# Kernel tuning notes

Hardware: AMD Instinct MI355X
Metric: run time of the kernel (lower is better)

## Reference

```python
import jax, jax.numpy as jnp
import numpy as np

B = 2; L = 64; HOP = 256; T = L * HOP
IN_CH = 101; INNER = 128; COND = 81
NBLOCK = 2; LAYERS = 5; K = 3; KH = 64
COUT = 2 * INNER
KCH = INNER * COUT * K * LAYERS   # 491520
BCH = COUT * LAYERS               # 1280


def setup_inputs() -> dict:
    key = jax.random.key(0)
    ks = jax.random.split(key, 12)
    n = lambda k, s, sc: jax.random.normal(k, s, jnp.float32) * sc
    return {
        "x": n(ks[0], (B, IN_CH, T), 1.0),
        "c": n(ks[1], (B, COND, L), 1.0),
        "fc_W": n(ks[2], (INNER, IN_CH), 0.1),
        "fc_b": jnp.zeros((INNER,), jnp.float32),
        "inp_W": n(ks[3], (NBLOCK, KH, COND, 5), 0.05),
        "inp_b": jnp.zeros((NBLOCK, KH), jnp.float32),
        "res1_W": n(ks[4], (NBLOCK, KH, KH), 0.1),
        "res1_b": jnp.zeros((NBLOCK, KH), jnp.float32),
        "res2_W": n(ks[5], (NBLOCK, KH, KH), 0.1),
        "res2_b": jnp.zeros((NBLOCK, KH), jnp.float32),
        "kern_W": n(ks[6], (NBLOCK, KCH, KH), 0.02),
        "kern_b": jnp.zeros((NBLOCK, KCH), jnp.float32),
        "biasc_W": n(ks[7], (NBLOCK, BCH, KH), 0.02),
        "biasc_b": jnp.zeros((NBLOCK, BCH), jnp.float32),
        "lc1_W": n(ks[8], (INNER, INNER), 0.08),
        "lc1_b": jnp.zeros((INNER,), jnp.float32),
        "lc2_W": n(ks[9], (1, INNER), 0.08),
        "lc2_b": jnp.zeros((1,), jnp.float32),
    }


def _conv1x1(x, W, b):
    return jnp.einsum('oc,bcl->bol', W, x) + b[None, :, None]


def _conv5(x, W, b):
    y = jax.lax.conv_general_dilated(x, W, (1,), [(2, 2)],
                                     dimension_numbers=('NCH', 'OIH', 'NCH'))
    return y + b[None, :, None]


def _lrelu(x):
    return jnp.where(x >= 0, x, 0.1 * x)


def _kernel_predictor(c, iW, ib, r1W, r1b, r2W, r2b, kW, kb, bW, bb):
    h = _lrelu(_conv5(c, iW, ib))
    h = h + _conv1x1(_lrelu(_conv1x1(h, r1W, r1b)), r2W, r2b)
    k = _conv1x1(h, kW, kb)   # (B, KCH, L)
    bb_ = _conv1x1(h, bW, bb)  # (B, BCH, L)
    Bn, _, Ln = c.shape
    kernels = k.reshape(Bn, LAYERS, INNER, COUT, K, Ln)
    bias = bb_.reshape(Bn, LAYERS, COUT, Ln)
    return kernels, bias


def _lvc(x, kernel, bias, dilation, hop):
    # x: (B, Cin, T); kernel: (B, Cin, Cout, K, L); bias: (B, Cout, L)
    Bn, Cin, Tn = x.shape
    _, _, O, Kn, Ln = kernel.shape
    p = dilation * (Kn - 1) // 2
    xp = jnp.pad(x, ((0, 0), (0, 0), (p, p)))
    win = hop + 2 * p
    # per-window gather (unfold over time with stride hop)
    idx = (jnp.arange(Ln) * hop)[:, None] + jnp.arange(win)[None, :]
    xw = xp[:, :, idx]
    m = win // dilation                                  # hop/d + (K-1)
    xt = xw.reshape(Bn, Cin, Ln, m, dilation).transpose(0, 1, 2, 4, 3)  # (B,Cin,L,d,m)
    S = hop // dilation
    idx2 = jnp.arange(S)[:, None] + jnp.arange(Kn)[None, :]  # (S, K) sliding taps
    xu = xt[..., idx2]                                   # (B, Cin, L, d, S, K)
    o = jnp.einsum('bildsk,biokl->bolsd', xu, kernel)
    o = o + bias[:, :, :, None, None]
    return o.reshape(Bn, O, Tn)


def _lvc_block(x, c, iW, ib, r1W, r1b, r2W, r2b, kW, kb, bW, bb):
    kernels, bias = _kernel_predictor(c, iW, ib, r1W, r1b, r2W, r2b, kW, kb, bW, bb)
    for i in range(LAYERS):
        d = 2 ** i  # max 16 < hop, so hop<dilation branch never triggers
        y = _lvc(x, kernels[:, i], bias[:, i], d, HOP)
        x = jax.nn.sigmoid(y[:, :INNER]) * jnp.tanh(y[:, INNER:])
    return x


def reference(x, c, fc_W, fc_b, inp_W, inp_b, res1_W, res1_b, res2_W, res2_b,
              kern_W, kern_b, biasc_W, biasc_b, lc1_W, lc1_b, lc2_W, lc2_b):
    h = _conv1x1(x, fc_W, fc_b)
    for n_ in range(NBLOCK):
        y = _lvc_block(h, c, inp_W[n_], inp_b[n_], res1_W[n_], res1_b[n_],
                       res2_W[n_], res2_b[n_], kern_W[n_], kern_b[n_],
                       biasc_W[n_], biasc_b[n_])
        h = y if n_ == 0 else h + y
    h = jnp.maximum(h, 0.0)
    h = _conv1x1(h, lc1_W, lc1_b)
    h = jnp.maximum(h, 0.0)
    h = _conv1x1(h, lc2_W, lc2_b)
    return h
```

## Files before the change

kernel.cpp:

```cpp
#include <hip/hip_runtime.h>
#include <math.h>

#define BB     2
#define LSEG   64
#define HOP    256
#define TT     (LSEG*HOP)
#define IN_CH  101
#define INNER  128
#define COND   81
#define LAYERS 5
#define KTAP   3
#define KH     64
#define COUT   256
#define RPL    (INNER*COUT*KTAP)
#define KCH    (RPL*LAYERS)
#define BCH    (COUT*LAYERS)
#define NBL    (BB*LSEG)
#define XS     36

typedef _Float16 f16;
typedef _Float16 f16x2 __attribute__((ext_vector_type(2)));
typedef _Float16 f16x8 __attribute__((ext_vector_type(8)));
typedef float    f32x4 __attribute__((ext_vector_type(4)));

__global__ __launch_bounds__(256) void k_fc(const float* __restrict__ x,
                                            const float* __restrict__ W,
                                            const float* __restrict__ bias,
                                            f16* __restrict__ out) {
    int half = blockIdx.x & 1;
    int g = (blockIdx.x >> 1)*256 + threadIdx.x;
    int b = g / TT, t = g % TT;
    float xv[IN_CH];
    const float* xp = x + (size_t)b*IN_CH*TT + t;
#pragma unroll
    for (int c = 0; c < IN_CH; ++c) xv[c] = xp[(size_t)c*TT];
    f16* op = out + (size_t)b*INNER*TT + t;
    int o0 = half*64;
    for (int o = o0; o < o0 + 64; ++o) {
        const float* wr = W + o*IN_CH;
        float a0 = bias[o], a1 = 0.f, a2 = 0.f, a3 = 0.f;
#pragma unroll
        for (int c = 0; c + 3 < IN_CH; c += 4) {
            a0 += wr[c]*xv[c]; a1 += wr[c+1]*xv[c+1];
            a2 += wr[c+2]*xv[c+2]; a3 += wr[c+3]*xv[c+3];
        }
        a0 += wr[100]*xv[100];
        op[(size_t)o*TT] = (f16)((a0+a1)+(a2+a3));
    }
}

__global__ __launch_bounds__(256) void k_h1(const float* __restrict__ cc,
                                            const float* __restrict__ iW,
                                            const float* __restrict__ ib,
                                            float* __restrict__ h1buf) {
    int og = blockIdx.x & 7;
    int bp = blockIdx.x >> 3;
    int b  = bp & 1;
    int n  = bp >> 1;
    __shared__ float cL[COND*LSEG];
    __shared__ float wL[8*COND*5];
    int tid = threadIdx.x;
    for (int idx = tid; idx < COND*LSEG; idx += 256)
        cL[idx] = cc[(size_t)b*COND*LSEG + idx];
    const float* wsrc = iW + (size_t)n*KH*COND*5 + (size_t)og*8*COND*5;
    for (int idx = tid; idx < 8*COND*5; idx += 256)
        wL[idx] = wsrc[idx];
    __syncthreads();
#pragma unroll
    for (int rep = 0; rep < 2; ++rep) {
        int idx = rep*256 + tid;
        int ol = idx >> 6, l = idx & 63;
        int o  = og*8 + ol;
        float acc = ib[n*KH + o];
        const float* wrow = wL + ol*COND*5;
        for (int i = 0; i < COND; ++i) {
            const float* crow = cL + i*LSEG;
            const float* w5 = wrow + i*5;
#pragma unroll
            for (int k = 0; k < 5; ++k) {
                int ll = l + k - 2;
                if (ll >= 0 && ll < LSEG) acc += crow[ll]*w5[k];
            }
        }
        h1buf[(((size_t)(n*BB + b))*KH + o)*LSEG + l] = acc >= 0.f ? acc : 0.1f*acc;
    }
}

__global__ __launch_bounds__(256) void k_h2t(const float* __restrict__ h1buf,
                                             const float* __restrict__ r1W,
                                             const float* __restrict__ r1b,
                                             const float* __restrict__ r2W,
                                             const float* __restrict__ r2b,
                                             float* __restrict__ h2buf,
                                             f16* __restrict__ h2h) {
    int b = blockIdx.x & 1;
    int n = blockIdx.x >> 1;
    __shared__ float h1L[KH*LSEG];
    __shared__ float t1L[KH*LSEG];
    __shared__ float wL[KH*KH];
    int tid = threadIdx.x;
    const float* h1src = h1buf + ((size_t)(n*BB + b))*KH*LSEG;
    for (int idx = tid; idx < KH*LSEG; idx += 256)
        h1L[idx] = h1src[idx];
    for (int idx = tid; idx < KH*KH; idx += 256)
        wL[idx] = r1W[(size_t)n*KH*KH + idx];
    __syncthreads();
#pragma unroll
    for (int rep = 0; rep < 16; ++rep) {
        int idx = rep*256 + tid;
        int o = idx >> 6, l = idx & 63;
        float acc = r1b[n*KH + o];
        const float* wr = wL + o*KH;
#pragma unroll
        for (int i = 0; i < KH; ++i) acc += wr[i]*h1L[i*LSEG + l];
        t1L[idx] = acc >= 0.f ? acc : 0.1f*acc;
    }
    __syncthreads();
    for (int idx = tid; idx < KH*KH; idx += 256)
        wL[idx] = r2W[(size_t)n*KH*KH + idx];
    __syncthreads();
#pragma unroll
    for (int rep = 0; rep < 16; ++rep) {
        int idx = rep*256 + tid;
        int o = idx >> 6, l = idx & 63;
        float acc = r2b[n*KH + o];
        const float* wr = wL + o*KH;
#pragma unroll
        for (int i = 0; i < KH; ++i) acc += wr[i]*t1L[i*LSEG + l];
        float h2 = h1L[o*LSEG + l] + acc;
        size_t row = (size_t)n*NBL + b*LSEG + l;
        h2buf[row*KH + o] = h2;
        h2h  [row*KH + o] = (f16)h2;
    }
}

__global__ __launch_bounds__(256) void k_biash(const float* __restrict__ bW,
                                               const float* __restrict__ bb,
                                               const float* __restrict__ h2buf,
                                               float* __restrict__ biasbuf) {
    int tg = blockIdx.x*256 + threadIdx.x;
    int n  = __builtin_amdgcn_readfirstlane(tg / (BB*BCH));
    int rem = tg - n*(BB*BCH);
    int b  = __builtin_amdgcn_readfirstlane(rem / BCH);
    int rb = rem % BCH;
    float w[KH];
    const float4* wp = (const float4*)(bW + ((size_t)n*BCH + rb)*KH);
#pragma unroll
    for (int q = 0; q < KH/4; ++q) {
        float4 v = wp[q];
        w[4*q] = v.x; w[4*q+1] = v.y; w[4*q+2] = v.z; w[4*q+3] = v.w;
    }
    float bv = bb[n*BCH + rb];
    for (int l = 0; l < LSEG; ++l) {
        size_t row = (size_t)n*NBL + b*LSEG + l;
        const float* h2 = h2buf + row*KH;
        float a0 = bv, a1 = 0.f, a2 = 0.f, a3 = 0.f;
#pragma unroll
        for (int j = 0; j < KH; j += 4) {
            a0 += w[j]*h2[j]; a1 += w[j+1]*h2[j+1];
            a2 += w[j+2]*h2[j+2]; a3 += w[j+3]*h2[j+3];
        }
        biasbuf[row*BCH + rb] = (a0+a1)+(a2+a3);
    }
}

__global__ __launch_bounds__(256) void k_gen(const float* __restrict__ kW,
                                             const float* __restrict__ kb,
                                             const f16*   __restrict__ h2h,
                                             f16*         __restrict__ kbuf) {
    int o2  = blockIdx.x & 127;
    int tmp = blockIdx.x >> 7;
    int tap = tmp % 3;
    int tmp2 = tmp / 3;
    int lay = tmp2 % 5;
    int n   = tmp2 / 5;
    int c   = threadIdx.x & 127;
    int oh  = threadIdx.x >> 7;
    int o   = o2 + (oh << 7);
    size_t r = (size_t)lay*RPL + (size_t)((c*COUT + o)*KTAP + tap);
    f16x2 wh[32];
    const float4* wp = (const float4*)(kW + ((size_t)n*KCH + r)*KH);
#pragma unroll
    for (int q = 0; q < 16; ++q) {
        float4 v = wp[q];
        wh[2*q]   = f16x2{(f16)v.x, (f16)v.y};
        wh[2*q+1] = f16x2{(f16)v.z, (f16)v.w};
    }
    float kbv = kb[(size_t)n*KCH + r];
    int op = 2*o2 + oh;
    size_t obase = (size_t)op*384 + (size_t)tap*128 + c;
    f16* kout = kbuf + ((size_t)(n*LAYERS + lay)*NBL)*RPL + obase;
    const uint* h2p = (const uint*)(h2h + (size_t)n*NBL*KH);
#pragma unroll 2
    for (int bl = 0; bl < NBL; ++bl) {
        const uint* hr = h2p + bl*32;
        float a0 = kbv, a1 = 0.f, a2 = 0.f, a3 = 0.f;
#pragma unroll
        for (int q = 0; q < 8; ++q) {
            a0 = __builtin_amdgcn_fdot2(wh[4*q],   __builtin_bit_cast(f16x2, hr[4*q]),   a0, false);
            a1 = __builtin_amdgcn_fdot2(wh[4*q+1], __builtin_bit_cast(f16x2, hr[4*q+1]), a1, false);
            a2 = __builtin_amdgcn_fdot2(wh[4*q+2], __builtin_bit_cast(f16x2, hr[4*q+2]), a2, false);
            a3 = __builtin_amdgcn_fdot2(wh[4*q+3], __builtin_bit_cast(f16x2, hr[4*q+3]), a3, false);
        }
        kout[(size_t)bl*RPL] = (f16)((a0+a1)+(a2+a3));
    }
}

template<int DIL>
__global__ __launch_bounds__(256) void k_lvc(const f16* __restrict__ xin,
                                             const f16* __restrict__ kbuf,
                                             const float* __restrict__ biasbuf,
                                             f16* __restrict__ xout,
                                             int layerIdx) {
    constexpr int WIN = 256 + 2*DIL;
    int wg  = blockIdx.x;
    int o0  = (wg & 3)*64;
    int l   = (wg >> 2) & 63;
    int b   = wg >> 8;
    int bl  = b*LSEG + l;
    int tid = threadIdx.x;
    int w   = tid >> 6;
    int lane = tid & 63;
    int quad = lane >> 4;
    int n16  = lane & 15;
    int wo = (w & 1)*32;
    int wt = (w >> 1)*128;

    __shared__ f16 As[3*64*XS];
    __shared__ f16 xwin[288*XS];

    const float* bias_l = biasbuf + (size_t)bl*BCH + layerIdx*COUT;
    f32x4 acc[2][8];
#pragma unroll
    for (int j = 0; j < 2; ++j) {
        int g0 = (o0 + wo + j*16 + quad*4) >> 1;
        f32x4 ini;
        ini[0] = bias_l[g0];       ini[1] = bias_l[g0 + 128];
        ini[2] = bias_l[g0 + 1];   ini[3] = bias_l[g0 + 1 + 128];
#pragma unroll
        for (int tt = 0; tt < 8; ++tt) acc[j][tt] = ini;
    }

    const f16* xb = xin + (size_t)b*INNER*TT;
    const f16* kbl = kbuf + (size_t)bl*RPL + (size_t)o0*384;
    int o_l = tid >> 2, q4 = tid & 3;
    int gt0 = l*256 - DIL;

    for (int cb = 0; cb < 4; ++cb) {
        for (int cc = w; cc < 32; cc += 4) {
            const f16* src = xb + (size_t)(cb*32 + cc)*TT;
#pragma unroll
            for (int tw0 = 0; tw0 < WIN; tw0 += 64) {
                int tw = tw0 + lane;
                if (tw < WIN) {
                    int gt = gt0 + tw;
                    f16 v = ((unsigned)gt < (unsigned)TT) ? src[gt] : (f16)0.f;
                    xwin[tw*XS + cc] = v;
                }
            }
        }
#pragma unroll
        for (int tap = 0; tap < 3; ++tap) {
            f16x8 v = *(const f16x8*)&kbl[(size_t)o_l*384 + tap*128 + cb*32 + q4*8];
            *(f16x8*)&As[(tap*64 + o_l)*XS + q4*8] = v;
        }
        __syncthreads();
#pragma unroll
        for (int tap = 0; tap < 3; ++tap) {
            f16x8 af0 = *(const f16x8*)&As[(tap*64 + wo + n16)*XS + quad*8];
            f16x8 af1 = *(const f16x8*)&As[(tap*64 + wo + 16 + n16)*XS + quad*8];
#pragma unroll
            for (int tt = 0; tt < 8; ++tt) {
                int trow = wt + tt*16 + n16 + tap*DIL;
                f16x8 bf = *(const f16x8*)&xwin[trow*XS + quad*8];
                acc[0][tt] = __builtin_amdgcn_mfma_f32_16x16x32_f16(af0, bf, acc[0][tt], 0, 0, 0);
                acc[1][tt] = __builtin_amdgcn_mfma_f32_16x16x32_f16(af1, bf, acc[1][tt], 0, 0, 0);
            }
        }
        __syncthreads();
    }
    f16* ob = xout + (size_t)b*INNER*TT + l*256;
#pragma unroll
    for (int j = 0; j < 2; ++j) {
        int g0 = (o0 + wo + j*16 + quad*4) >> 1;
#pragma unroll
        for (int tt = 0; tt < 8; ++tt) {
            int tloc = wt + tt*16 + n16;
            f32x4 a = acc[j][tt];
            float s0  = 1.f/(1.f + __expf(-a[0]));
            float th0 = 2.f/(1.f + __expf(-2.f*a[1])) - 1.f;
            float s1  = 1.f/(1.f + __expf(-a[2]));
            float th1 = 2.f/(1.f + __expf(-2.f*a[3])) - 1.f;
            ob[(size_t)g0*TT + tloc]     = (f16)(s0*th0);
            ob[(size_t)(g0+1)*TT + tloc] = (f16)(s1*th1);
        }
    }
}

__global__ __launch_bounds__(256) void k_head(const f16* __restrict__ y0,
                                              const f16* __restrict__ y1,
                                              const float* __restrict__ W1,
                                              const float* __restrict__ b1,
                                              const float* __restrict__ W2,
                                              const float* __restrict__ b2,
                                              float* __restrict__ out) {
    int b    = blockIdx.x >> 8;
    int tseg = (blockIdx.x & 255)*64;
    int tid  = threadIdx.x;
    int w    = tid >> 6;
    int lane = tid & 63;
    int t    = tseg + lane;
    __shared__ float red[4][64];

    float h[INNER];
    const f16* p0 = y0 + (size_t)b*INNER*TT + t;
    const f16* p1 = y1 + (size_t)b*INNER*TT + t;
#pragma unroll
    for (int c = 0; c < INNER; ++c) {
        float v = (float)p0[(size_t)c*TT] + (float)p1[(size_t)c*TT];
        h[c] = v > 0.f ? v : 0.f;
    }
    float part = 0.f;
    int oBase = w*32;
    for (int oi = 0; oi < 32; ++oi) {
        int o = oBase + oi;
        const float* wr = W1 + o*INNER;
        float z0 = b1[o], z1 = 0.f, z2 = 0.f, z3 = 0.f;
#pragma unroll
        for (int c = 0; c < INNER; c += 4) {
            z0 += wr[c]*h[c];   z1 += wr[c+1]*h[c+1];
            z2 += wr[c+2]*h[c+2]; z3 += wr[c+3]*h[c+3];
        }
        float z = (z0+z1)+(z2+z3);
        z = z > 0.f ? z : 0.f;
        part += W2[o]*z;
    }
    red[w][lane] = part;
    __syncthreads();
    if (w == 0) {
        float acc = b2[0] + red[0][lane] + red[1][lane] + red[2][lane] + red[3][lane];
        out[(size_t)b*TT + t] = acc;
    }
}

extern "C" void kernel_launch(void* const* d_in, const int* in_sizes, int n_in,
                              void* d_out, int out_size, void* d_ws, size_t ws_size,
                              hipStream_t stream) {
    const float* x    = (const float*)d_in[0];
    const float* c    = (const float*)d_in[1];
    const float* fcW  = (const float*)d_in[2];
    const float* fcb  = (const float*)d_in[3];
    const float* inpW = (const float*)d_in[4];
    const float* inpb = (const float*)d_in[5];
    const float* r1W  = (const float*)d_in[6];
    const float* r1b  = (const float*)d_in[7];
    const float* r2W  = (const float*)d_in[8];
    const float* r2b  = (const float*)d_in[9];
    const float* kW   = (const float*)d_in[10];
    const float* kb   = (const float*)d_in[11];
    const float* bW   = (const float*)d_in[12];
    const float* bb   = (const float*)d_in[13];
    const float* l1W  = (const float*)d_in[14];
    const float* l1b  = (const float*)d_in[15];
    const float* l2W  = (const float*)d_in[16];
    const float* l2b  = (const float*)d_in[17];

    float* ws = (float*)d_ws;
    float* h2buf   = ws;
    float* biasbuf = h2buf + (size_t)2*NBL*KH;
    float* h1buf   = biasbuf + (size_t)2*NBL*BCH;
    f16*   h2h     = (f16*)(h1buf + (size_t)2*BB*KH*LSEG);
    f16*   bufA    = h2h + (size_t)2*NBL*KH;
    f16*   bufB    = bufA + (size_t)BB*INNER*TT;
    f16*   bufC    = bufB + (size_t)BB*INNER*TT;
    f16*   kbuf    = bufC + (size_t)BB*INNER*TT;

    k_fc<<<BB*TT/256*2, 256, 0, stream>>>(x, fcW, fcb, bufA);

    k_h1<<<32, 256, 0, stream>>>(c, inpW, inpb, h1buf);
    k_h2t<<<4, 256, 0, stream>>>(h1buf, r1W, r1b, r2W, r2b, h2buf, h2h);
    k_biash<<<20, 256, 0, stream>>>(bW, bb, h2buf, biasbuf);
    k_gen<<<2*LAYERS*3*128, 256, 0, stream>>>(kW, kb, h2h, kbuf);

    for (int n = 0; n < 2; ++n) {
        const float* bias_n = biasbuf + (size_t)n*NBL*BCH;
        f16* pin = (n == 0) ? bufA : bufB;
        f16* s0  = (n == 0) ? bufB : bufC;
        f16* s1  = (n == 0) ? bufC : bufA;
        f16* cin = pin;
        for (int i = 0; i < LAYERS; ++i) {
            const f16* kslice = kbuf + (size_t)(n*LAYERS + i)*NBL*RPL;
            f16* cout_ = (i % 2 == 0) ? s0 : s1;
            switch (i) {
                case 0: k_lvc<1> <<<BB*LSEG*4, 256, 0, stream>>>(cin, kslice, bias_n, cout_, i); break;
                case 1: k_lvc<2> <<<BB*LSEG*4, 256, 0, stream>>>(cin, kslice, bias_n, cout_, i); break;
                case 2: k_lvc<4> <<<BB*LSEG*4, 256, 0, stream>>>(cin, kslice, bias_n, cout_, i); break;
                case 3: k_lvc<8> <<<BB*LSEG*4, 256, 0, stream>>>(cin, kslice, bias_n, cout_, i); break;
                case 4: k_lvc<16><<<BB*LSEG*4, 256, 0, stream>>>(cin, kslice, bias_n, cout_, i); break;
            }
            cin = cout_;
        }
    }
    k_head<<<BB*TT/64, 256, 0, stream>>>(bufB, bufC, l1W, l1b, l2W, l2b, (float*)d_out);
}
```

Before: 1.176 ms.

## Use MFMA in kernel generator and split LVC time segments in half

The kernel-predictor generation GEMM (kern_W times h2) is rewritten from per-thread fdot2 loops into MFMA 16x16x32 tiles, with each block covering all 128 input channels for one output/tap and writing packed f16x4 stores. Separately, the LVC kernel now processes half of a 256-sample hop per workgroup, doubling the grid to 1024 blocks and halving accumulators and shared window size. This should improve occupancy and parallelism, at the cost of reloading the kernel slice from global memory twice per segment.

```diff
diff --git a/kernel.cpp b/kernel.cpp
--- a/kernel.cpp
+++ b/kernel.cpp
@@ -20,6 +20,7 @@
 
 typedef _Float16 f16;
 typedef _Float16 f16x2 __attribute__((ext_vector_type(2)));
+typedef _Float16 f16x4 __attribute__((ext_vector_type(4)));
 typedef _Float16 f16x8 __attribute__((ext_vector_type(8)));
 typedef float    f32x4 __attribute__((ext_vector_type(4)));
 
@@ -168,41 +169,61 @@
                                              const float* __restrict__ kb,
                                              const f16*   __restrict__ h2h,
                                              f16*         __restrict__ kbuf) {
-    int o2  = blockIdx.x & 127;
-    int tmp = blockIdx.x >> 7;
-    int tap = tmp % 3;
-    int tmp2 = tmp / 3;
-    int lay = tmp2 % 5;
-    int n   = tmp2 / 5;
-    int c   = threadIdx.x & 127;
-    int oh  = threadIdx.x >> 7;
-    int o   = o2 + (oh << 7);
-    size_t r = (size_t)lay*RPL + (size_t)((c*COUT + o)*KTAP + tap);
-    f16x2 wh[32];
-    const float4* wp = (const float4*)(kW + ((size_t)n*KCH + r)*KH);
-#pragma unroll
-    for (int q = 0; q < 16; ++q) {
-        float4 v = wp[q];
-        wh[2*q]   = f16x2{(f16)v.x, (f16)v.y};
-        wh[2*q+1] = f16x2{(f16)v.z, (f16)v.w};
-    }
-    float kbv = kb[(size_t)n*KCH + r];
-    int op = 2*o2 + oh;
-    size_t obase = (size_t)op*384 + (size_t)tap*128 + c;
+    int o   = blockIdx.x & 255;
+    int tmp = blockIdx.x >> 8;
+    int tap = tmp % 3;  tmp /= 3;
+    int lay = tmp % 5;
+    int n   = tmp / 5;
+    int lane = threadIdx.x & 63;
+    int wm   = threadIdx.x >> 6;
+    int n16  = lane & 15;
+    int quad = lane >> 4;
+
+    size_t rbase = (size_t)n*KCH + (size_t)lay*RPL;
+    const f16* h2b = h2h + (size_t)n*NBL*KH;
+
+    f16x8 afr[2][2];
+#pragma unroll
+    for (int j = 0; j < 2; ++j) {
+        int c = wm*32 + j*16 + n16;
+        const float* arow = kW + (rbase + (size_t)(c*COUT + o)*KTAP + tap)*KH;
+#pragma unroll
+        for (int ks = 0; ks < 2; ++ks) {
+            float4 v0 = *(const float4*)(arow + ks*32 + quad*8);
+            float4 v1 = *(const float4*)(arow + ks*32 + quad*8 + 4);
+            afr[j][ks] = f16x8{(f16)v0.x,(f16)v0.y,(f16)v0.z,(f16)v0.w,
+                               (f16)v1.x,(f16)v1.y,(f16)v1.z,(f16)v1.w};
+        }
+    }
+    f32x4 bini[2];
+#pragma unroll
+    for (int j = 0; j < 2; ++j) {
+#pragma unroll
+        for (int r = 0; r < 4; ++r) {
+            int c = wm*32 + j*16 + quad*4 + r;
+            bini[j][r] = kb[rbase + (size_t)(c*COUT + o)*KTAP + tap];
+        }
+    }
+    int op = (o < 128) ? 2*o : 2*(o-128) + 1;
+    size_t obase = (size_t)op*384 + (size_t)tap*128;
     f16* kout = kbuf + ((size_t)(n*LAYERS + lay)*NBL)*RPL + obase;
-    const uint* h2p = (const uint*)(h2h + (size_t)n*NBL*KH);
+
 #pragma unroll 2
-    for (int bl = 0; bl < NBL; ++bl) {
-        const uint* hr = h2p + bl*32;
-        float a0 = kbv, a1 = 0.f, a2 = 0.f, a3 = 0.f;
-#pragma unroll
-        for (int q = 0; q < 8; ++q) {
-            a0 = __builtin_amdgcn_fdot2(wh[4*q],   __builtin_bit_cast(f16x2, hr[4*q]),   a0, false);
-            a1 = __builtin_amdgcn_fdot2(wh[4*q+1], __builtin_bit_cast(f16x2, hr[4*q+1]), a1, false);
-            a2 = __builtin_amdgcn_fdot2(wh[4*q+2], __builtin_bit_cast(f16x2, hr[4*q+2]), a2, false);
-            a3 = __builtin_amdgcn_fdot2(wh[4*q+3], __builtin_bit_cast(f16x2, hr[4*q+3]), a3, false);
-        }
-        kout[(size_t)bl*RPL] = (f16)((a0+a1)+(a2+a3));
+    for (int t = 0; t < 8; ++t) {
+        int bl = t*16 + n16;
+        const f16* brow = h2b + (size_t)bl*KH;
+        f16x8 bf0 = *(const f16x8*)(brow + quad*8);
+        f16x8 bf1 = *(const f16x8*)(brow + 32 + quad*8);
+        f32x4 acc0 = bini[0], acc1 = bini[1];
+        acc0 = __builtin_amdgcn_mfma_f32_16x16x32_f16(afr[0][0], bf0, acc0, 0, 0, 0);
+        acc0 = __builtin_amdgcn_mfma_f32_16x16x32_f16(afr[0][1], bf1, acc0, 0, 0, 0);
+        acc1 = __builtin_amdgcn_mfma_f32_16x16x32_f16(afr[1][0], bf0, acc1, 0, 0, 0);
+        acc1 = __builtin_amdgcn_mfma_f32_16x16x32_f16(afr[1][1], bf1, acc1, 0, 0, 0);
+        int c0 = wm*32 + quad*4;
+        *(f16x4*)(kout + (size_t)bl*RPL + c0) =
+            f16x4{(f16)acc0[0],(f16)acc0[1],(f16)acc0[2],(f16)acc0[3]};
+        *(f16x4*)(kout + (size_t)bl*RPL + c0 + 16) =
+            f16x4{(f16)acc1[0],(f16)acc1[1],(f16)acc1[2],(f16)acc1[3]};
     }
 }
 
@@ -212,11 +233,12 @@
                                              const float* __restrict__ biasbuf,
                                              f16* __restrict__ xout,
                                              int layerIdx) {
-    constexpr int WIN = 256 + 2*DIL;
+    constexpr int WIN = 128 + 2*DIL;
     int wg  = blockIdx.x;
     int o0  = (wg & 3)*64;
-    int l   = (wg >> 2) & 63;
-    int b   = wg >> 8;
+    int th  = (wg >> 2) & 1;
+    int l   = (wg >> 3) & 63;
+    int b   = wg >> 9;
     int bl  = b*LSEG + l;
     int tid = threadIdx.x;
     int w   = tid >> 6;
@@ -224,13 +246,13 @@
     int quad = lane >> 4;
     int n16  = lane & 15;
     int wo = (w & 1)*32;
-    int wt = (w >> 1)*128;
+    int wt = (w >> 1)*64;
 
     __shared__ f16 As[3*64*XS];
-    __shared__ f16 xwin[288*XS];
+    __shared__ f16 xwin[WIN*XS];
 
     const float* bias_l = biasbuf + (size_t)bl*BCH + layerIdx*COUT;
-    f32x4 acc[2][8];
+    f32x4 acc[2][4];
 #pragma unroll
     for (int j = 0; j < 2; ++j) {
         int g0 = (o0 + wo + j*16 + quad*4) >> 1;
@@ -238,13 +260,13 @@
         ini[0] = bias_l[g0];       ini[1] = bias_l[g0 + 128];
         ini[2] = bias_l[g0 + 1];   ini[3] = bias_l[g0 + 1 + 128];
 #pragma unroll
-        for (int tt = 0; tt < 8; ++tt) acc[j][tt] = ini;
+        for (int tt = 0; tt < 4; ++tt) acc[j][tt] = ini;
     }
 
     const f16* xb = xin + (size_t)b*INNER*TT;
     const f16* kbl = kbuf + (size_t)bl*RPL + (size_t)o0*384;
     int o_l = tid >> 2, q4 = tid & 3;
-    int gt0 = l*256 - DIL;
+    int gt0 = l*256 + th*128 - DIL;
 
     for (int cb = 0; cb < 4; ++cb) {
         for (int cc = w; cc < 32; cc += 4) {
@@ -270,7 +292,7 @@
             f16x8 af0 = *(const f16x8*)&As[(tap*64 + wo + n16)*XS + quad*8];
             f16x8 af1 = *(const f16x8*)&As[(tap*64 + wo + 16 + n16)*XS + quad*8];
 #pragma unroll
-            for (int tt = 0; tt < 8; ++tt) {
+            for (int tt = 0; tt < 4; ++tt) {
                 int trow = wt + tt*16 + n16 + tap*DIL;
                 f16x8 bf = *(const f16x8*)&xwin[trow*XS + quad*8];
                 acc[0][tt] = __builtin_amdgcn_mfma_f32_16x16x32_f16(af0, bf, acc[0][tt], 0, 0, 0);
@@ -279,12 +301,12 @@
         }
         __syncthreads();
     }
-    f16* ob = xout + (size_t)b*INNER*TT + l*256;
+    f16* ob = xout + (size_t)b*INNER*TT + l*256 + th*128;
 #pragma unroll
     for (int j = 0; j < 2; ++j) {
         int g0 = (o0 + wo + j*16 + quad*4) >> 1;
 #pragma unroll
-        for (int tt = 0; tt < 8; ++tt) {
+        for (int tt = 0; tt < 4; ++tt) {
             int tloc = wt + tt*16 + n16;
             f32x4 a = acc[j][tt];
             float s0  = 1.f/(1.f + __expf(-a[0]));
@@ -380,7 +402,7 @@
     k_h1<<<32, 256, 0, stream>>>(c, inpW, inpb, h1buf);
     k_h2t<<<4, 256, 0, stream>>>(h1buf, r1W, r1b, r2W, r2b, h2buf, h2h);
     k_biash<<<20, 256, 0, stream>>>(bW, bb, h2buf, biasbuf);
-    k_gen<<<2*LAYERS*3*128, 256, 0, stream>>>(kW, kb, h2h, kbuf);
+    k_gen<<<2*LAYERS*3*256, 256, 0, stream>>>(kW, kb, h2h, kbuf);
 
     for (int n = 0; n < 2; ++n) {
         const float* bias_n = biasbuf + (size_t)n*NBL*BCH;
@@ -392,11 +414,11 @@
             const f16* kslice = kbuf + (size_t)(n*LAYERS + i)*NBL*RPL;
             f16* cout_ = (i % 2 == 0) ? s0 : s1;
             switch (i) {
-                case 0: k_lvc<1> <<<BB*LSEG*4, 256, 0, stream>>>(cin, kslice, bias_n, cout_, i); break;
-                case 1: k_lvc<2> <<<BB*LSEG*4, 256, 0, stream>>>(cin, kslice, bias_n, cout_, i); break;
-                case 2: k_lvc<4> <<<BB*LSEG*4, 256, 0, stream>>>(cin, kslice, bias_n, cout_, i); break;
-                case 3: k_lvc<8> <<<BB*LSEG*4, 256, 0, stream>>>(cin, kslice, bias_n, cout_, i); break;
-                case 4: k_lvc<16><<<BB*LSEG*4, 256, 0, stream>>>(cin, kslice, bias_n, cout_, i); break;
+                case 0: k_lvc<1> <<<BB*LSEG*2*4, 256, 0, stream>>>(cin, kslice, bias_n, cout_, i); break;
+                case 1: k_lvc<2> <<<BB*LSEG*2*4, 256, 0, stream>>>(cin, kslice, bias_n, cout_, i); break;
+                case 2: k_lvc<4> <<<BB*LSEG*2*4, 256, 0, stream>>>(cin, kslice, bias_n, cout_, i); break;
+                case 3: k_lvc<8> <<<BB*LSEG*2*4, 256, 0, stream>>>(cin, kslice, bias_n, cout_, i); break;
+                case 4: k_lvc<16><<<BB*LSEG*2*4, 256, 0, stream>>>(cin, kslice, bias_n, cout_, i); break;
             }
             cin = cout_;
         }
```

Result: faster. 1.139 ms (-3.2%).
